# Kernel tuning notes

Measured on AMD Instinct MI355X. Metric: run time of the kernel, lower is better.

Reference implementation:

```python
import jax, jax.numpy as jnp
import numpy as np

# ---- fixed acquisition / imaging constants (from init_kwargs) ----
C = 1540.0            # speed of sound (m/s)
FS = 20e6             # sampling rate (Hz)
DR = C / FS           # meters per sample (dr)
R0 = 0.0              # range offset (data_span[0]=0)
TIK = 0.1             # tikhonov regularization
DB_MIN = -60.0
XPX, ZPX = 200, 200
N_ELEM, N_ENC, N_SAMP = 64, 32, 2048
PITCH = 0.3e-3


def setup_inputs() -> dict:
    key = jax.random.key(0)
    k1, k2, k3, k4 = jax.random.split(key, 4)
    datas = jax.random.normal(k1, (2, N_ELEM, N_SAMP, N_ELEM), dtype=jnp.float32)
    locs = jax.random.normal(k2, (2, 8, 3), dtype=jnp.float32)
    delays = 3.0 * jax.random.normal(k3, (N_ENC, N_ELEM), dtype=jnp.float32)   # samples
    weights = jax.random.normal(k4, (N_ENC, N_ELEM), dtype=jnp.float32)
    # calc_delays_beamforming: one-way path length (m) from each element to each pixel
    xe = (np.arange(N_ELEM) - (N_ELEM - 1) / 2.0) * PITCH            # element x (m)
    x = np.linspace(-15.0, 15.0, XPX) / 1000.0                        # pixel x (m)
    z = np.linspace(10.0, 40.0, ZPX) / 1000.0                         # pixel z (m)
    Z, X = np.meshgrid(z, x, indexing='ij')                           # [ZPX, XPX]
    d = np.sqrt((X[None] - xe[:, None, None]) ** 2 + Z[None] ** 2)    # [E, ZPX, XPX]
    bf_delays = jnp.asarray(d.reshape(N_ELEM, -1), dtype=jnp.float32) # [E, P]
    return {"datas": datas, "locs": locs, "delays": delays,
            "weights": weights, "bf_delays": bf_delays}


def _hilbert(x, axis):
    n = x.shape[axis]
    h = np.zeros(n, dtype=np.float32)
    h[0] = 1.0
    h[n // 2] = 1.0
    h[1:n // 2] = 2.0
    shape = [1] * x.ndim
    shape[axis] = n
    return jnp.fft.ifft(jnp.fft.fft(x, axis=axis) * jnp.asarray(h).reshape(shape), axis=axis)


def reference(datas, locs, delays, weights, bf_delays):
    B, T, S, R = datas.shape
    # ---- calc_H: frequency-domain encoding matrix H[f, tx, enc] ----
    f = jnp.fft.fftfreq(S).astype(jnp.float32)                                 # cycles/sample
    phase = jnp.exp(-2j * jnp.pi * f[:, None, None] * delays.T[None, :, :])    # [S, T, E]
    H = weights.T[None, :, :].astype(jnp.complex64) * phase                    # [S, T, E]
    # ---- calc_Hinv_tikhonov: per-freq (H^H H + lam I)^-1 H^H  -> [S, E, T] ----
    Hh = jnp.conj(H).transpose(0, 2, 1)                                        # [S, E, T]
    A = jnp.einsum('fet,ftd->fed', Hh, H) + TIK * jnp.eye(H.shape[2], dtype=jnp.complex64)
    Hinv = jnp.linalg.solve(A, Hh)                                             # [S, E, T]
    # ---- encode / decode (freq-domain matmuls, batched over B) ----
    F = jnp.fft.fft(datas, axis=2)                                             # [B, T, S, R]
    rf_enc = jnp.real(jnp.fft.ifft(jnp.einsum('fte,btfr->befr', H, F), axis=2))  # [B, E, S, R]
    F2 = jnp.fft.fft(rf_enc, axis=2)
    rf_dec = jnp.real(jnp.fft.ifft(jnp.einsum('fet,befr->btfr', Hinv, F2), axis=2))  # [B, T, S, R]
    iq = _hilbert(rf_dec, axis=2)                                              # analytic signal
    # ---- BeamformAD: delay-and-sum with linear interpolation ----
    d_rx = bf_delays                                                           # [R, P]
    P = d_rx.shape[1]

    def beamform_one(iq_b):                                                    # iq_b [T, S, R]
        iq_rs = iq_b.transpose(0, 2, 1)                                        # [T, R, S]
        def step(acc, xs):
            iq_t, d_t = xs                                                     # [R, S], [P]
            t = (d_t[None, :] + d_rx - R0) / DR                                # [R, P] fractional sample
            i0 = jnp.floor(t)
            frac = (t - i0)
            i0i = i0.astype(jnp.int32)
            valid = (i0i >= 0) & (i0i < S - 1)
            i0c = jnp.clip(i0i, 0, S - 2)
            v0 = jnp.take_along_axis(iq_t, i0c, axis=1)
            v1 = jnp.take_along_axis(iq_t, i0c + 1, axis=1)
            val = jnp.where(valid, v0 * (1.0 - frac) + v1 * frac, 0.0)
            return acc + val.sum(0), None
        acc0 = jnp.zeros((P,), dtype=iq_b.dtype)
        img, _ = jax.lax.scan(step, acc0, (iq_rs, d_rx))
        return img

    img = jax.vmap(beamform_one)(iq)                                           # [B, P]
    pred = jnp.abs(img).reshape(B, ZPX, XPX) + 1e-15
    mx = jnp.max(pred, axis=(1, 2), keepdims=True)
    out = jnp.clip(20.0 * jnp.log10(pred / mx), DB_MIN, 0.0)
    return out
```

## Files before the change

### kernel.cpp

```cpp
#include <hip/hip_runtime.h>
#include <math.h>

#define S_LEN 2048
#define K_HALF 1025
#define N_T 64
#define N_E 32
#define N_R 64
#define N_P 40000
#define XPX 200
#define ZPX 200
#define WIN0 256
#define WIN_LEN 1024
#define W_LDS 96
#define RSTRIDE 100
#define TWO_PI 6.283185307179586f
#define PITCH 0.3e-3f
#define PXSTEP (30.0f/199.0f*1e-3f)

__device__ __forceinline__ float2 cmul(float2 a, float2 b) {
  return make_float2(a.x*b.x - a.y*b.y, a.x*b.y + a.y*b.x);
}

__global__ void k_fft_fwd(const float* __restrict__ db, float2* __restrict__ F) {
  __shared__ float2 xs[S_LEN];
  __shared__ float2 tw[S_LEN/2];
  int t  = blockIdx.x;
  int rq = blockIdx.y;
  int tid = threadIdx.x;
  for (int j = tid; j < S_LEN/2; j += 256) {
    float ang = -TWO_PI * (float)j / (float)S_LEN;
    tw[j] = make_float2(__cosf(ang), __sinf(ang));
  }
  int r0 = rq * 2;
  const float2* src = (const float2*)(db + (size_t)t * S_LEN * N_R + r0);
  for (int n = tid; n < S_LEN; n += 256) {
    int rn = __brev((unsigned)n) >> 21;
    xs[rn] = src[(size_t)n * (N_R/2)];
  }
  __syncthreads();
  for (int h = 1; h <= 256; h <<= 2) {
    int tsA = 1024 / h, tsB = 512 / h;
    for (int idx = tid; idx < 512; idx += 256) {
      int j = idx & (h - 1);
      int i0 = ((idx & ~(h - 1)) << 2) | j;
      float2 wA = tw[j * tsA];
      float2 wB = tw[j * tsB];
      float2 a = xs[i0], b = xs[i0 + h], c = xs[i0 + 2*h], d = xs[i0 + 3*h];
      float2 tb = cmul(wA, b), td = cmul(wA, d);
      float2 u0 = make_float2(a.x+tb.x, a.y+tb.y);
      float2 u1 = make_float2(a.x-tb.x, a.y-tb.y);
      float2 u2 = make_float2(c.x+td.x, c.y+td.y);
      float2 u3 = make_float2(c.x-td.x, c.y-td.y);
      float2 v2 = cmul(wB, u2);
      float2 v3t = cmul(wB, u3);
      float2 v3 = make_float2(v3t.y, -v3t.x);
      xs[i0]       = make_float2(u0.x+v2.x, u0.y+v2.y);
      xs[i0 + 2*h] = make_float2(u0.x-v2.x, u0.y-v2.y);
      xs[i0 + h]   = make_float2(u1.x+v3.x, u1.y+v3.y);
      xs[i0 + 3*h] = make_float2(u1.x-v3.x, u1.y-v3.y);
    }
    __syncthreads();
  }
  for (int idx = tid; idx < 1024; idx += 256) {
    float2 w = tw[idx];
    float2 a = xs[idx], b = xs[idx + 1024];
    float2 tt = cmul(w, b);
    xs[idx]        = make_float2(a.x+tt.x, a.y+tt.y);
    xs[idx + 1024] = make_float2(a.x-tt.x, a.y-tt.y);
  }
  __syncthreads();
  float2* F0 = F + ((size_t)(r0+0) * N_T + t) * K_HALF;
  float2* F1 = F + ((size_t)(r0+1) * N_T + t) * K_HALF;
  for (int k = tid; k < K_HALF; k += 256) {
    int m = (S_LEN - k) & (S_LEN - 1);
    float2 s = xs[k], sm = xs[m];
    F0[k] = make_float2(0.5f*(s.x + sm.x), 0.5f*(s.y - sm.y));
    F1[k] = make_float2(0.5f*(s.y + sm.y), 0.5f*(sm.x - s.x));
  }
}

__global__ __launch_bounds__(256) void k_solveM(const float* __restrict__ delays,
                                                const float* __restrict__ weights,
                                                float2* __restrict__ Hinv,
                                                float2* __restrict__ Hg) {
  __shared__ float2 Hs[N_T][N_E+1];
  __shared__ float2 AX[N_E][97];
  __shared__ float2 g[N_E];
  __shared__ float2 invds[N_E];
  int k = blockIdx.x;
  int tid = threadIdx.x;
  float fk = (float)k / (float)S_LEN;
  for (int i = tid; i < N_T*N_E; i += 256) {
    int t = i & 63, e = i >> 6;
    float d = delays[e*N_T + t], w = weights[e*N_T + t];
    float ang = -TWO_PI * fk * d;
    Hs[t][e] = make_float2(w*__cosf(ang), w*__sinf(ang));
  }
  __syncthreads();
  {
    float2* Hp = Hg + (size_t)k * (N_T*N_E);
    for (int i = tid; i < N_T*N_E; i += 256) {
      int t = i >> 5, e = i & 31;
      Hp[i] = Hs[t][e];
    }
  }
  for (int s = tid; s < 528; s += 256) {
    int dd = (int)((sqrtf(8.f*(float)s + 1.f) - 1.f) * 0.5f);
    while (dd*(dd+1)/2 > s) --dd;
    while ((dd+1)*(dd+2)/2 <= s) ++dd;
    int e = s - dd*(dd+1)/2;
    float ar = 0.f, ai = 0.f;
    for (int tt = 0; tt < N_T; ++tt) {
      float2 he = Hs[tt][e], hd = Hs[tt][dd];
      ar += he.x*hd.x + he.y*hd.y;
      ai += he.x*hd.y - he.y*hd.x;
    }
    if (e == dd) ar += 0.1f;
    AX[e][dd] = make_float2(ar, ai);
  }
  __syncthreads();
  for (int idx = tid; idx < N_E*N_E; idx += 256) {
    int e = idx >> 5, dd = idx & 31;
    if (e > dd) {
      float2 u = AX[dd][e];
      AX[e][dd] = make_float2(u.x, -u.y);
    }
  }
  for (int idx = tid; idx < N_E*N_T; idx += 256) {
    int e = idx >> 6, t = idx & 63;
    float2 h = Hs[t][e];
    AX[e][32 + t] = make_float2(h.x, -h.y);
  }
  __syncthreads();
  int j = tid >> 3;
  int cb = tid & 7;
  for (int i = 0; i < N_E; ++i) {
    if (tid < N_E) {
      float2 dg = AX[i][i];
      float rden = 1.f / (dg.x*dg.x + dg.y*dg.y);
      float2 iv = make_float2(dg.x*rden, -dg.y*rden);
      g[tid] = cmul(AX[tid][i], iv);
      if (tid == 0) invds[i] = iv;
    }
    __syncthreads();
    if (j != i) {
      float2 gj = g[j];
      int cbase = cb * 12;
      #pragma unroll
      for (int u = 0; u < 12; ++u) {
        int c = cbase + u;
        float2 piv = AX[i][c];
        float2 v = AX[j][c];
        AX[j][c] = make_float2(v.x - (gj.x*piv.x - gj.y*piv.y),
                               v.y - (gj.x*piv.y + gj.y*piv.x));
      }
    }
    __syncthreads();
  }
  bool edge = (k == 0) || (k == S_LEN/2);
  float coef = edge ? (1.0f/(float)S_LEN) : (2.0f/(float)S_LEN);
  float2* Op = Hinv + (size_t)k * (N_E*N_T);
  for (int idx = tid; idx < N_E*N_T; idx += 256) {
    int e = idx >> 6, t = idx & 63;
    float2 v = cmul(AX[e][32+t], invds[e]);
    Op[idx] = make_float2(v.x*coef, v.y*coef);
  }
}

__global__ __launch_bounds__(256) void k_combine2(const float2* __restrict__ F,
                                                  const float2* __restrict__ Hinv,
                                                  const float2* __restrict__ Hg,
                                                  float2* __restrict__ Yk) {
  __shared__ float2 Fs[N_T][N_R];
  __shared__ float2 HG[N_T*N_E];
  int wg = blockIdx.x;
  int xcd = wg & 7, ci = wg >> 3;
  int k = (xcd == 0) ? ci : (129 + (xcd - 1) * 128 + ci);
  int tid = threadIdx.x;
  for (int i = tid; i < N_T*N_R; i += 256) {
    int t = i >> 6, r = i & 63;
    Fs[t][r] = F[((size_t)(r*N_T + t)) * K_HALF + k];
  }
  {
    const float2* Hp = Hg + (size_t)k * (N_T*N_E);
    for (int i = tid; i < N_T*N_E; i += 256)
      HG[i] = Hp[i];
  }
  __syncthreads();
  bool edge = (k == 0) || (k == S_LEN/2);
  int lane = tid & 63;
  int w = __builtin_amdgcn_readfirstlane(tid >> 6);
  float2 ga[8];
  #pragma unroll
  for (int i = 0; i < 8; ++i) ga[i] = make_float2(0.f, 0.f);
  for (int t = 0; t < N_T; ++t) {
    float2 f = Fs[t][lane];
    #pragma unroll
    for (int i = 0; i < 8; ++i) {
      float2 h = HG[t*N_E + w*8 + i];
      ga[i].x += h.x*f.x - h.y*f.y;
      ga[i].y += h.x*f.y + h.y*f.x;
    }
  }
  __syncthreads();
  if (edge) {
    #pragma unroll
    for (int i = 0; i < 8; ++i) ga[i].y = 0.f;
  }
  #pragma unroll
  for (int i = 0; i < 8; ++i)
    HG[(w*8 + i)*N_R + lane] = ga[i];
  __syncthreads();
  const float2* Hk = Hinv + (size_t)k * (N_E*N_T) + w*16;
  float2 acc[16];
  #pragma unroll
  for (int i = 0; i < 16; ++i) acc[i] = make_float2(0.f, 0.f);
  for (int e = 0; e < N_E; ++e) {
    float2 f = HG[e*N_R + lane];
    const float2* hrow = Hk + e*N_T;
    #pragma unroll
    for (int i = 0; i < 16; ++i) {
      float2 m = hrow[i];
      acc[i].x += m.x*f.x - m.y*f.y;
      acc[i].y += m.x*f.y + m.y*f.x;
    }
  }
  float2* Yp = Yk + (size_t)k * (N_T*N_R) + w*16*N_R + lane;
  #pragma unroll
  for (int i = 0; i < 16; ++i)
    Yp[(size_t)i * N_R] = make_float2(acc[i].x, edge ? 0.f : acc[i].y);
}

__global__ void k_ifft(const float2* __restrict__ Yk, float2* __restrict__ iq) {
  __shared__ float2 xsA[S_LEN];
  __shared__ float2 xsB[S_LEN];
  __shared__ float2 tw[S_LEN/2];
  int wg = blockIdx.x;
  int j0 = ((wg & 7) * 256 + (wg >> 3)) * 2;
  int tid = threadIdx.x;
  for (int q = tid; q < S_LEN/2; q += 256) {
    float ang = TWO_PI * (float)q / (float)S_LEN;
    tw[q] = make_float2(__cosf(ang), __sinf(ang));
  }
  for (int n = tid; n < S_LEN; n += 256) {
    int rn = __brev((unsigned)n) >> 21;
    float2 a, b;
    if (n < K_HALF) {
      float4 v = *reinterpret_cast<const float4*>(Yk + (size_t)n * (N_T*N_R) + j0);
      a = make_float2(v.x, v.y);
      b = make_float2(v.z, v.w);
    } else {
      a = make_float2(0.f, 0.f);
      b = make_float2(0.f, 0.f);
    }
    xsA[rn] = a;
    xsB[rn] = b;
  }
  __syncthreads();
  for (int h = 1; h <= 256; h <<= 2) {
    int tsA = 1024 / h, tsB = 512 / h;
    for (int idx = tid; idx < 512; idx += 256) {
      int j = idx & (h - 1);
      int i0 = ((idx & ~(h - 1)) << 2) | j;
      float2 wA = tw[j * tsA];
      float2 wB = tw[j * tsB];
      {
        float2 a = xsA[i0], b = xsA[i0 + h], c = xsA[i0 + 2*h], d = xsA[i0 + 3*h];
        float2 tb = cmul(wA, b), td = cmul(wA, d);
        float2 u0 = make_float2(a.x+tb.x, a.y+tb.y);
        float2 u1 = make_float2(a.x-tb.x, a.y-tb.y);
        float2 u2 = make_float2(c.x+td.x, c.y+td.y);
        float2 u3 = make_float2(c.x-td.x, c.y-td.y);
        float2 v2 = cmul(wB, u2);
        float2 v3t = cmul(wB, u3);
        float2 v3 = make_float2(-v3t.y, v3t.x);
        xsA[i0]       = make_float2(u0.x+v2.x, u0.y+v2.y);
        xsA[i0 + 2*h] = make_float2(u0.x-v2.x, u0.y-v2.y);
        xsA[i0 + h]   = make_float2(u1.x+v3.x, u1.y+v3.y);
        xsA[i0 + 3*h] = make_float2(u1.x-v3.x, u1.y-v3.y);
      }
      {
        float2 a = xsB[i0], b = xsB[i0 + h], c = xsB[i0 + 2*h], d = xsB[i0 + 3*h];
        float2 tb = cmul(wA, b), td = cmul(wA, d);
        float2 u0 = make_float2(a.x+tb.x, a.y+tb.y);
        float2 u1 = make_float2(a.x-tb.x, a.y-tb.y);
        float2 u2 = make_float2(c.x+td.x, c.y+td.y);
        float2 u3 = make_float2(c.x-td.x, c.y-td.y);
        float2 v2 = cmul(wB, u2);
        float2 v3t = cmul(wB, u3);
        float2 v3 = make_float2(-v3t.y, v3t.x);
        xsB[i0]       = make_float2(u0.x+v2.x, u0.y+v2.y);
        xsB[i0 + 2*h] = make_float2(u0.x-v2.x, u0.y-v2.y);
        xsB[i0 + h]   = make_float2(u1.x+v3.x, u1.y+v3.y);
        xsB[i0 + 3*h] = make_float2(u1.x-v3.x, u1.y-v3.y);
      }
    }
    __syncthreads();
  }
  float2* rowA = iq + (size_t)j0 * WIN_LEN;
  float2* rowB = iq + (size_t)(j0+1) * WIN_LEN;
  for (int idx = tid; idx < 1024; idx += 256) {
    float2 w = tw[idx];
    {
      float2 a = xsA[idx], b = xsA[idx + 1024];
      float2 tt = cmul(w, b);
      if (idx >= WIN0) rowA[idx - WIN0] = make_float2(a.x+tt.x, a.y+tt.y);
      else             rowA[idx + (1024 - WIN0)] = make_float2(a.x-tt.x, a.y-tt.y);
    }
    {
      float2 a = xsB[idx], b = xsB[idx + 1024];
      float2 tt = cmul(w, b);
      if (idx >= WIN0) rowB[idx - WIN0] = make_float2(a.x+tt.x, a.y+tt.y);
      else             rowB[idx + (1024 - WIN0)] = make_float2(a.x-tt.x, a.y-tt.y);
    }
  }
}

__global__ __launch_bounds__(256, 2) void k_beamform(const float2* __restrict__ iq,
                                                     float2* __restrict__ imgp) {
  __shared__ float winRe[N_R][RSTRIDE];
  __shared__ float winIm[N_R][RSTRIDE];
  __shared__ float basef[N_R];
  int wg = blockIdx.x;
  int tg = wg & 7;
  int bx = wg >> 3;
  int tid = threadIdx.x;
  int tx = tid & 15, tz = tid >> 4;
  int x = (bx % 13) * 16 + tx;
  int z = (bx / 13) * 16 + tz;
  bool ok = (x < XPX) && (z < ZPX);
  int p = z * XPX + x;
  const float invDR = (float)(20.0e6 / 1540.0);
  float xm = fmaf((float)x, PXSTEP, -15e-3f);
  float zm = fmaf((float)z, PXSTEP, 10e-3f);
  float z2 = zm * zm;
  float xm0 = fmaf((float)((bx % 13) * 16), PXSTEP, -15e-3f);
  float xm1 = xm0 + 15.f * PXSTEP;
  float zb0 = fmaf((float)((bx / 13) * 16), PXSTEP, 10e-3f);
  float zb2 = zb0 * zb0;
  float di[64];
  #pragma unroll
  for (int e = 0; e < 64; ++e) {
    float xe = ((float)e - 31.5f) * PITCH;
    float dx = xm - xe;
    di[e] = sqrtf(fmaf(dx, dx, z2)) * invDR;
  }
  int rrow = tid >> 2, sub = tid & 3;
  float xer = ((float)rrow - 31.5f) * PITCH;
  float dxr = fminf(fmaxf(xer, xm0), xm1) - xer;
  float minDR_r = sqrtf(fmaf(dxr, dxr, zb2)) * invDR;
  float ar = 0.f, ai = 0.f;
  #pragma unroll 1
  for (int t8 = 0; t8 < 8; ++t8) {
    int t = tg * 8 + t8;
    float xet = ((float)t - 31.5f) * PITCH;
    float dxt = fminf(fmaxf(xet, xm0), xm1) - xet;
    float minDT = sqrtf(fmaf(dxt, dxt, zb2)) * invDR;
    int base = (int)floorf(minDT + minDR_r) - 1;
    base = min(base, WIN0 + WIN_LEN - W_LDS);
    if (sub == 0) basef[rrow] = (float)base;
    const float2* rowp = iq + ((size_t)t * N_R + rrow) * WIN_LEN + (base - WIN0);
    #pragma unroll
    for (int jj = 0; jj < 12; ++jj) {
      int s = sub * 24 + jj * 2;
      float4 v = *reinterpret_cast<const float4*>(rowp + s);
      winRe[rrow][s]   = v.x;  winRe[rrow][s+1] = v.z;
      winIm[rrow][s]   = v.y;  winIm[rrow][s+1] = v.w;
    }
    __syncthreads();
    float dxT = xm - xet;
    float dti = sqrtf(fmaf(dxT, dxT, z2)) * invDR;
    #pragma unroll
    for (int r = 0; r < 64; ++r) {
      float rel = dti + di[r] - basef[r];
      int o = (int)rel;
      float fr = rel - (float)o;
      float re0 = winRe[r][o], re1 = winRe[r][o+1];
      float im0 = winIm[r][o], im1 = winIm[r][o+1];
      ar += re0 + fr * (re1 - re0);
      ai += im0 + fr * (im1 - im0);
    }
    __syncthreads();
  }
  if (ok) imgp[(size_t)tg * N_P + p] = make_float2(ar, ai);
}

__global__ void k_magred(const float2* __restrict__ imgp, float* __restrict__ mag) {
  int p = blockIdx.x*256 + threadIdx.x;
  if (p >= N_P) return;
  float ar = 0.f, ai = 0.f;
  #pragma unroll
  for (int g = 0; g < 8; ++g) {
    float2 v = imgp[(size_t)g * N_P + p];
    ar += v.x; ai += v.y;
  }
  mag[p] = sqrtf(ar*ar + ai*ai);
}

__global__ void k_max(const float* __restrict__ mag, float* __restrict__ mx) {
  __shared__ float red[256];
  int b = blockIdx.x, tid = threadIdx.x;
  float m = 0.f;
  for (int i = tid; i < N_P; i += 256) m = fmaxf(m, mag[(size_t)b*N_P + i]);
  red[tid] = m; __syncthreads();
  for (int s = 128; s > 0; s >>= 1) {
    if (tid < s) red[tid] = fmaxf(red[tid], red[tid+s]);
    __syncthreads();
  }
  if (tid == 0) mx[b] = red[0] + 1e-15f;
}

__global__ void k_final(const float* __restrict__ mag, const float* __restrict__ mx,
                        float* __restrict__ out) {
  int i = blockIdx.x*256 + threadIdx.x;
  if (i >= 2*N_P) return;
  int b = i / N_P;
  float v = (mag[i] + 1e-15f) / mx[b];
  float db = 20.f * log10f(v);
  out[i] = fminf(fmaxf(db, -60.f), 0.f);
}

extern "C" void kernel_launch(void* const* d_in, const int* in_sizes, int n_in,
                              void* d_out, int out_size, void* d_ws, size_t ws_size,
                              hipStream_t stream) {
  const float* datas   = (const float*)d_in[0];
  const float* delays  = (const float*)d_in[2];
  const float* weights = (const float*)d_in[3];
  float* out = (float*)d_out;
  char* ws = (char*)d_ws;

  size_t off = 0;
  float2* Hinv = (float2*)(ws + off); off += (size_t)K_HALF*N_E*N_T*sizeof(float2);
  float2* Hg   = (float2*)(ws + off); off += (size_t)K_HALF*N_T*N_E*sizeof(float2);
  float2* Yk   = (float2*)(ws + off); off += (size_t)K_HALF*N_T*N_R*sizeof(float2);
  float2* F    = (float2*)(ws + off); off += (size_t)N_R*N_T*K_HALF*sizeof(float2);
  float2* iq   = (float2*)F;
  float2* imgp = (float2*)(ws + off); off += (size_t)8*N_P*sizeof(float2);
  float*  mag  = (float*)(ws + off);  off += (size_t)2*N_P*sizeof(float);
  float*  mx   = (float*)(ws + off);  off += 256;

  k_solveM<<<dim3(K_HALF), dim3(256), 0, stream>>>(delays, weights, Hinv, Hg);
  for (int b = 0; b < 2; ++b) {
    const float* db = datas + (size_t)b * N_T * S_LEN * N_R;
    k_fft_fwd<<<dim3(64, 32), dim3(256), 0, stream>>>(db, F);
    k_combine2<<<dim3(K_HALF), dim3(256), 0, stream>>>(F, Hinv, Hg, Yk);
    k_ifft<<<dim3(N_T*N_R/2), dim3(256), 0, stream>>>(Yk, iq);
    k_beamform<<<dim3(1352), dim3(256), 0, stream>>>(iq, imgp);
    k_magred<<<dim3((N_P+255)/256), dim3(256), 0, stream>>>(imgp, mag + (size_t)b*N_P);
  }
  k_max<<<dim3(2), dim3(256), 0, stream>>>(mag, mx);
  k_final<<<dim3((2*N_P+255)/256), dim3(256), 0, stream>>>(mag, mx, out);
}
```

Baseline: 643.4 us.

## Transpose F and Yk layouts to move strided access between FFT and combine stages

Result: no change. 633.2 us (-1.6%).

```diff
diff --git a/kernel.cpp b/kernel.cpp
--- a/kernel.cpp
+++ b/kernel.cpp
@@ -69,13 +69,13 @@
     xs[idx + 1024] = make_float2(a.x-tt.x, a.y-tt.y);
   }
   __syncthreads();
-  float2* F0 = F + ((size_t)(r0+0) * N_T + t) * K_HALF;
-  float2* F1 = F + ((size_t)(r0+1) * N_T + t) * K_HALF;
+  float* Fp = (float*)(F + (size_t)t * N_R + r0);
   for (int k = tid; k < K_HALF; k += 256) {
     int m = (S_LEN - k) & (S_LEN - 1);
     float2 s = xs[k], sm = xs[m];
-    F0[k] = make_float2(0.5f*(s.x + sm.x), 0.5f*(s.y - sm.y));
-    F1[k] = make_float2(0.5f*(s.y + sm.y), 0.5f*(sm.x - s.x));
+    float4 v = make_float4(0.5f*(s.x + sm.x), 0.5f*(s.y - sm.y),
+                           0.5f*(s.y + sm.y), 0.5f*(sm.x - s.x));
+    *reinterpret_cast<float4*>(Fp + (size_t)k * (N_T*N_R*2)) = v;
   }
 }
 
@@ -177,9 +177,11 @@
   int xcd = wg & 7, ci = wg >> 3;
   int k = (xcd == 0) ? ci : (129 + (xcd - 1) * 128 + ci);
   int tid = threadIdx.x;
-  for (int i = tid; i < N_T*N_R; i += 256) {
-    int t = i >> 6, r = i & 63;
-    Fs[t][r] = F[((size_t)(r*N_T + t)) * K_HALF + k];
+  {
+    const float4* Fk = (const float4*)(F + (size_t)k * (N_T*N_R));
+    float4* FsL = (float4*)Fs;
+    for (int i = tid; i < N_T*N_R/2; i += 256)
+      FsL[i] = Fk[i];
   }
   {
     const float2* Hp = Hg + (size_t)k * (N_T*N_E);
@@ -225,10 +227,10 @@
       acc[i].y += m.x*f.y + m.y*f.x;
     }
   }
-  float2* Yp = Yk + (size_t)k * (N_T*N_R) + w*16*N_R + lane;
+  float2* Yp = Yk + (size_t)(w*16*N_R + lane) * K_HALF + k;
   #pragma unroll
   for (int i = 0; i < 16; ++i)
-    Yp[(size_t)i * N_R] = make_float2(acc[i].x, edge ? 0.f : acc[i].y);
+    Yp[(size_t)i * (N_R*K_HALF)] = make_float2(acc[i].x, edge ? 0.f : acc[i].y);
 }
 
 __global__ void k_ifft(const float2* __restrict__ Yk, float2* __restrict__ iq) {
@@ -242,17 +244,12 @@
     float ang = TWO_PI * (float)q / (float)S_LEN;
     tw[q] = make_float2(__cosf(ang), __sinf(ang));
   }
+  const float2* rowAg = Yk + (size_t)j0 * K_HALF;
+  const float2* rowBg = rowAg + K_HALF;
   for (int n = tid; n < S_LEN; n += 256) {
     int rn = __brev((unsigned)n) >> 21;
-    float2 a, b;
-    if (n < K_HALF) {
-      float4 v = *reinterpret_cast<const float4*>(Yk + (size_t)n * (N_T*N_R) + j0);
-      a = make_float2(v.x, v.y);
-      b = make_float2(v.z, v.w);
-    } else {
-      a = make_float2(0.f, 0.f);
-      b = make_float2(0.f, 0.f);
-    }
+    float2 a = make_float2(0.f, 0.f), b = make_float2(0.f, 0.f);
+    if (n < K_HALF) { a = rowAg[n]; b = rowBg[n]; }
     xsA[rn] = a;
     xsB[rn] = b;
   }
@@ -432,8 +429,8 @@
   size_t off = 0;
   float2* Hinv = (float2*)(ws + off); off += (size_t)K_HALF*N_E*N_T*sizeof(float2);
   float2* Hg   = (float2*)(ws + off); off += (size_t)K_HALF*N_T*N_E*sizeof(float2);
-  float2* Yk   = (float2*)(ws + off); off += (size_t)K_HALF*N_T*N_R*sizeof(float2);
-  float2* F    = (float2*)(ws + off); off += (size_t)N_R*N_T*K_HALF*sizeof(float2);
+  float2* Yk   = (float2*)(ws + off); off += (size_t)(N_T*N_R)*K_HALF*sizeof(float2);
+  float2* F    = (float2*)(ws + off); off += (size_t)K_HALF*N_T*N_R*sizeof(float2);
   float2* iq   = (float2*)F;
   float2* imgp = (float2*)(ws + off); off += (size_t)8*N_P*sizeof(float2);
   float*  mag  = (float*)(ws + off);  off += (size_t)2*N_P*sizeof(float);
```
